# Kernel optimization log

Hardware: AMD Instinct MI355X
Metric: run time of the kernel (lower is better)

## Reference

```python
import jax, jax.numpy as jnp
import numpy as np

N = 1_000_000   # total nodes
B = 20_000      # number of graphs (segments)
V = 100_000     # item vocab (rows of feat table)
D = 128         # input_dim
H = 128         # hidden_dim
O = 256         # output_dim
EPS = 1e-5


def setup_inputs() -> dict:
    key = jax.random.key(0)
    ks = jax.random.split(key, 10)
    feat = jax.random.normal(ks[0], (V, D), dtype=jnp.float32)
    iid = jax.random.randint(ks[1], (N,), 0, V)
    segment_ids = jnp.sort(jax.random.randint(ks[2], (N,), 0, B))
    last_nodes = jax.random.randint(ks[3], (B,), 0, N)
    s = 1.0 / np.sqrt(D)
    gamma = jnp.ones((D,), jnp.float32)
    beta = jnp.zeros((D,), jnp.float32)
    W_u = jax.random.uniform(ks[4], (D, H), jnp.float32, -s, s)
    W_v = jax.random.uniform(ks[5], (D, H), jnp.float32, -s, s)
    b_v = jax.random.uniform(ks[6], (H,), jnp.float32, -s, s)
    w_e = jax.random.uniform(ks[7], (H,), jnp.float32, -1.0 / np.sqrt(H), 1.0 / np.sqrt(H))
    W_out = jax.random.uniform(ks[8], (D, O), jnp.float32, -s, s)
    return {"feat": feat, "iid": iid, "segment_ids": segment_ids,
            "last_nodes": last_nodes, "gamma": gamma, "beta": beta,
            "W_u": W_u, "W_v": W_v, "b_v": b_v, "w_e": w_e, "W_out": W_out}


def reference(feat, iid, segment_ids, last_nodes, gamma, beta, W_u, W_v, b_v, w_e, W_out):
    # gather per-node features from item table
    x = feat[iid]                                  # [N, D]
    # BatchNorm1d (training mode: batch statistics, biased var)
    mean = jnp.mean(x, axis=0)
    var = jnp.mean((x - mean) ** 2, axis=0)
    x = (x - mean) * jax.lax.rsqrt(var + EPS) * gamma + beta
    # projections
    feat_u = x @ W_u                               # [N, H]
    feat_v = x[last_nodes] @ W_v + b_v             # [B, H]
    e = jax.nn.sigmoid(feat_u + feat_v[segment_ids]) @ w_e   # [N]
    # segment softmax over per-graph node segments
    e_max = jax.ops.segment_max(e, segment_ids, num_segments=B)
    ex = jnp.exp(e - e_max[segment_ids])
    denom = jax.ops.segment_sum(ex, segment_ids, num_segments=B)
    alpha = ex / denom[segment_ids]                # [N]
    # weighted segment sum, then output projection
    rst = jax.ops.segment_sum(x * alpha[:, None], segment_ids, num_segments=B)  # [B, D]
    return rst @ W_out                             # [B, O]
```

## Files before the change

kernel.cpp:

```cpp
#include <hip/hip_runtime.h>

typedef __attribute__((ext_vector_type(8))) short short8;
typedef __attribute__((ext_vector_type(4))) float floatx4;
typedef __attribute__((ext_vector_type(4))) int intx4;

static __device__ __forceinline__ unsigned short f2bf(float x) {
    unsigned int u = __float_as_uint(x);
    u += 0x7fffu + ((u >> 16) & 1u);
    return (unsigned short)(u >> 16);
}

template <int CTRL>
static __device__ __forceinline__ float dpp_add(float x) {
    int v = __builtin_amdgcn_update_dpp(0, __float_as_int(x), CTRL, 0xf, 0xf, true);
    return x + __int_as_float(v);
}

__global__ void k_hist(const int* __restrict__ iid, int* __restrict__ counts, int N) {
    int n = blockIdx.x * blockDim.x + threadIdx.x;
    if (n < N) atomicAdd(&counts[iid[n]], 1);
}

__global__ __launch_bounds__(256) void k_cvtstats(const float* __restrict__ feat,
                                                  const int* __restrict__ counts,
                                                  unsigned short* __restrict__ featb,
                                                  float* __restrict__ dsum, float* __restrict__ dsumsq,
                                                  int V) {
    int tid = threadIdx.x;
    int r2 = tid >> 7, d = tid & 127;
    float s = 0.f, qa = 0.f;
    for (int vp = blockIdx.x; vp * 2 < V; vp += gridDim.x) {
        int v = vp * 2 + r2;
        if (v >= V) continue;
        float f = feat[(size_t)v * 128 + d];
        featb[(size_t)v * 128 + d] = f2bf(f);
        float c = (float)counts[v];
        if (c != 0.f) { s += c * f; qa += c * f * f; }
    }
    __shared__ float red[256];
    red[tid] = s; __syncthreads();
    if (tid < 128) atomicAdd(&dsum[d], red[tid] + red[tid + 128]);
    __syncthreads();
    red[tid] = qa; __syncthreads();
    if (tid < 128) atomicAdd(&dsumsq[d], red[tid] + red[tid + 128]);
}

__global__ __launch_bounds__(128) void k_affine(const float* __restrict__ sum,
                                                const float* __restrict__ sumsq,
                                                const float* __restrict__ gamma,
                                                const float* __restrict__ beta,
                                                float* __restrict__ scale, float* __restrict__ shift,
                                                float invN) {
    int d = threadIdx.x;
    float mean = sum[d] * invN;
    float var  = sumsq[d] * invN - mean * mean;
    float sc   = gamma[d] * rsqrtf(var + 1e-5f);
    scale[d] = sc;
    shift[d] = beta[d] - mean * sc;
}

__global__ __launch_bounds__(128) void k_prep(const float* __restrict__ Wu, const float* __restrict__ Wv,
                                              const float* __restrict__ bv,
                                              const float* __restrict__ scale, const float* __restrict__ shift,
                                              unsigned short* __restrict__ wut, float* __restrict__ wvs,
                                              float* __restrict__ cbias) {
    int h = blockIdx.x, d = threadIdx.x;
    float sc = scale[d], sh = shift[d];
    float wu = Wu[d * 128 + h], wv = Wv[d * 128 + h];
    wut[h * 128 + d] = f2bf(sc * wu);
    wvs[d * 128 + h] = sc * wv;
    __shared__ float red[128];
    red[d] = sh * (wu + wv);
    __syncthreads();
    for (int off = 64; off > 0; off >>= 1) {
        if (d < off) red[d] += red[d + off];
        __syncthreads();
    }
    if (d == 0) cbias[h] = bv[h] + red[0];
}

__global__ __launch_bounds__(128) void k_fv(const float* __restrict__ feat, const int* __restrict__ iid,
                                            const int* __restrict__ last, const float* __restrict__ wvs,
                                            const float* __restrict__ cbias, float* __restrict__ fv,
                                            int B) {
    const int GPB = 8;
    int b0 = blockIdx.x * GPB;
    int h = threadIdx.x;
    __shared__ float sx[GPB][128];
    for (int g = 0; g < GPB; ++g) {
        int b = b0 + g;
        if (b < B) {
            int row = iid[last[b]];
            sx[g][h] = feat[(size_t)row * 128 + h];
        }
    }
    __syncthreads();
    float acc[GPB];
#pragma unroll
    for (int g = 0; g < GPB; ++g) acc[g] = 0.f;
    for (int d = 0; d < 128; ++d) {
        float w = wvs[d * 128 + h];
#pragma unroll
        for (int g = 0; g < GPB; ++g) acc[g] += sx[g][d] * w;
    }
    float c = cbias[h];
    for (int g = 0; g < GPB; ++g)
        if (b0 + g < B) fv[(size_t)(b0 + g) * 128 + h] = acc[g] + c;
}

__global__ __launch_bounds__(256, 4) void k_main(
        const unsigned short* __restrict__ featb, const int* __restrict__ iid,
        const int* __restrict__ seg, const unsigned short* __restrict__ wut,
        const float* __restrict__ fv, const float* __restrict__ we_g,
        float* __restrict__ rstAcc, float* __restrict__ den,
        int N, int B, int numTiles) {
    __shared__ unsigned short sA[2][64 * 128];
    __shared__ int   sSeg[2][64];
    __shared__ float sFv[2][4][128];
    __shared__ float sEp[4][64];

    int tid = threadIdx.x;
    int wv = tid >> 6, lane = tid & 63, q = lane >> 4, c = lane & 15;
    int p2 = lane & 15;
    int rowbase = wv * 16 + (lane >> 4);

    short8 bfr[2][4];
    float we2[2];
#pragma unroll
    for (int t = 0; t < 2; ++t) {
        int h = (2 * wv + t) * 16 + c;
        we2[t] = we_g[h];
#pragma unroll
        for (int kc = 0; kc < 4; ++kc)
            bfr[t][kc] = *(const short8*)(wut + h * 128 + kc * 32 + q * 8);
    }

    if (blockIdx.x >= numTiles) return;

    int iidR[4]; int segR; float2 fvR;
    auto loadRegs = [&](int T) {
        int n0 = T << 6;
#pragma unroll
        for (int k = 0; k < 4; ++k)
            iidR[k] = iid[min(n0 + rowbase + 4 * k, N - 1)];
        segR = seg[min(n0 + (tid & 63), N - 1)];
        int s0 = __builtin_amdgcn_readfirstlane(segR);
        int fvrow = min(s0 + (tid >> 6), B - 1);
        fvR = *(const float2*)(fv + (size_t)fvrow * 128 + ((tid << 1) & 127));
    };
    auto stage = [&](int buf) {
        unsigned short* sAb = &sA[buf][0];
#pragma unroll
        for (int k = 0; k < 4; ++k) {
            int row = rowbase + 4 * k;
            int j = (p2 & 8) | ((p2 & 7) ^ (row & 7));
            const unsigned short* g = featb + (size_t)iidR[k] * 128 + j * 8;
            __builtin_amdgcn_global_load_lds(
                (const __attribute__((address_space(1))) void*)g,
                (__attribute__((address_space(3))) void*)(sAb + wv * 2048 + k * 512),
                16, 0, 0);
        }
        if (tid < 64) sSeg[buf][tid] = segR;
        *(float2*)&sFv[buf][tid >> 6][(tid << 1) & 127] = fvR;
    };

    int T = blockIdx.x;
    loadRegs(T);
    stage(0);
    int cur = 0;

    for (;;) {
        int Tn = T + gridDim.x;
        bool hn = (Tn < numTiles);
        if (hn) loadRegs(Tn);
        __syncthreads();
        if (hn) stage(cur ^ 1);

        floatx4 acc[4][2];
#pragma unroll
        for (int mt = 0; mt < 4; ++mt)
#pragma unroll
            for (int t = 0; t < 2; ++t) acc[mt][t] = (floatx4)(0.f);
#pragma unroll
        for (int kc = 0; kc < 4; ++kc) {
            int jj = 4 * kc + q;
            int pofs = ((jj & 8) | ((jj & 7) ^ (c & 7))) * 8;
            short8 a0 = *(const short8*)&sA[cur][( 0 + c) * 128 + pofs];
            short8 a1 = *(const short8*)&sA[cur][(16 + c) * 128 + pofs];
            short8 a2 = *(const short8*)&sA[cur][(32 + c) * 128 + pofs];
            short8 a3 = *(const short8*)&sA[cur][(48 + c) * 128 + pofs];
#pragma unroll
            for (int t = 0; t < 2; ++t) {
                acc[0][t] = __builtin_amdgcn_mfma_f32_16x16x32_bf16(a0, bfr[t][kc], acc[0][t], 0, 0, 0);
                acc[1][t] = __builtin_amdgcn_mfma_f32_16x16x32_bf16(a1, bfr[t][kc], acc[1][t], 0, 0, 0);
                acc[2][t] = __builtin_amdgcn_mfma_f32_16x16x32_bf16(a2, bfr[t][kc], acc[2][t], 0, 0, 0);
                acc[3][t] = __builtin_amdgcn_mfma_f32_16x16x32_bf16(a3, bfr[t][kc], acc[3][t], 0, 0, 0);
            }
        }
        {
            int s0 = sSeg[cur][0];
            int h0 = wv * 32 + c;
#pragma unroll
            for (int mt = 0; mt < 4; ++mt)
#pragma unroll
                for (int r = 0; r < 4; ++r) {
                    int nl = mt * 16 + q * 4 + r;
                    int sg = sSeg[cur][nl];
                    int off = sg - s0;
                    float f0, f1;
                    if (off < 4) {
                        f0 = sFv[cur][off][h0];
                        f1 = sFv[cur][off][h0 + 16];
                    } else {
                        f0 = fv[((size_t)sg << 7) + h0];
                        f1 = fv[((size_t)sg << 7) + h0 + 16];
                    }
                    float u0 = acc[mt][0][r] + f0;
                    float u1 = acc[mt][1][r] + f1;
                    float p = we2[0] * __builtin_amdgcn_rcpf(1.f + __expf(-u0))
                            + we2[1] * __builtin_amdgcn_rcpf(1.f + __expf(-u1));
                    p = dpp_add<0xb1>(p);
                    p = dpp_add<0x4e>(p);
                    p = dpp_add<0x141>(p);
                    p = dpp_add<0x140>(p);
                    if (c == 0) sEp[wv][nl] = p;
                }
        }
        __syncthreads();

        {
            int n0 = T << 6;
            int nb = wv * 16;
            float exr[16];
#pragma unroll
            for (int jg = 0; jg < 4; ++jg) {
                floatx4 e0 = *(const floatx4*)&sEp[0][nb + jg * 4];
                floatx4 e1 = *(const floatx4*)&sEp[1][nb + jg * 4];
                floatx4 e2 = *(const floatx4*)&sEp[2][nb + jg * 4];
                floatx4 e3 = *(const floatx4*)&sEp[3][nb + jg * 4];
#pragma unroll
                for (int r = 0; r < 4; ++r) {
                    float s = e0[r] + e1[r] + e2[r] + e3[r];
                    exr[jg * 4 + r] = (n0 + nb + jg * 4 + r < N) ? __expf(s) : 0.f;
                }
            }
            int sgr[16];
#pragma unroll
            for (int jg = 0; jg < 4; ++jg)
                *(intx4*)&sgr[jg * 4] = *(const intx4*)&sSeg[cur][nb + jg * 4];

            int d0 = lane * 2;
            int jj = lane >> 2;
            int wsub = (lane & 3) * 4;
            const char* base = (const char*)&sA[cur][0];
            float a0 = 0.f, a1 = 0.f, dl = 0.f;
            int curseg = sgr[0];
#pragma unroll
            for (int j = 0; j < 16; ++j) {
                int row = nb + j;
                int sg = sgr[j];
                if (sg != curseg) {
                    atomicAdd(&rstAcc[(size_t)curseg * 128 + d0], a0);
                    atomicAdd(&rstAcc[(size_t)curseg * 128 + d0 + 1], a1);
                    if (lane == 0) atomicAdd(&den[curseg], dl);
                    a0 = a1 = dl = 0.f; curseg = sg;
                }
                int ch = (jj & 8) | ((jj & 7) ^ (row & 7));
                unsigned u = *(const unsigned*)(base + row * 256 + ch * 16 + wsub);
                float e = exr[j];
                a0 += e * __uint_as_float(u << 16);
                a1 += e * __uint_as_float(u & 0xffff0000u);
                dl += e;
            }
            atomicAdd(&rstAcc[(size_t)curseg * 128 + d0], a0);
            atomicAdd(&rstAcc[(size_t)curseg * 128 + d0 + 1], a1);
            if (lane == 0) atomicAdd(&den[curseg], dl);
        }

        if (!hn) break;
        T = Tn; cur ^= 1;
    }
}

__global__ __launch_bounds__(256) void k_out(const float* __restrict__ rstAcc,
                                             const float* __restrict__ den,
                                             const float* __restrict__ scale,
                                             const float* __restrict__ shift,
                                             const float* __restrict__ Wout,
                                             float* __restrict__ out, int B) {
    __shared__ float sT[128][36];
    __shared__ float sInv[32];
    int b0 = blockIdx.x * 32;
    int t = threadIdx.x;
    for (int i = 0; i < 16; ++i) {
        int idx = i * 256 + t;
        int r = idx >> 7, d = idx & 127;
        int b = min(b0 + r, B - 1);
        sT[d][r] = scale[d] * rstAcc[((size_t)b << 7) + d];
    }
    if (t < 32) {
        int b = min(b0 + t, B - 1);
        float dn = den[b];
        sInv[t] = (dn > 0.f) ? 1.f / dn : 0.f;
    }
    __syncthreads();
    float acc[32];
#pragma unroll
    for (int r = 0; r < 32; ++r) acc[r] = 0.f;
    float sb = 0.f;
    for (int dd = 0; dd < 128; ++dd) {
        float w = Wout[dd * 256 + t];
        sb += shift[dd] * w;
        const float4* row = (const float4*)&sT[dd][0];
#pragma unroll
        for (int r4 = 0; r4 < 8; ++r4) {
            float4 v = row[r4];
            acc[r4 * 4 + 0] += w * v.x;
            acc[r4 * 4 + 1] += w * v.y;
            acc[r4 * 4 + 2] += w * v.z;
            acc[r4 * 4 + 3] += w * v.w;
        }
    }
    for (int r = 0; r < 32; ++r)
        if (b0 + r < B) {
            float inv = sInv[r];
            out[(size_t)(b0 + r) * 256 + t] = acc[r] * inv + (inv != 0.f ? sb : 0.f);
        }
}

extern "C" void kernel_launch(void* const* d_in, const int* in_sizes, int n_in,
                              void* d_out, int out_size, void* d_ws, size_t ws_size,
                              hipStream_t stream) {
    const float* feat  = (const float*)d_in[0];
    const int*   iid   = (const int*)d_in[1];
    const int*   seg   = (const int*)d_in[2];
    const int*   last  = (const int*)d_in[3];
    const float* gamma = (const float*)d_in[4];
    const float* beta  = (const float*)d_in[5];
    const float* Wu    = (const float*)d_in[6];
    const float* Wv    = (const float*)d_in[7];
    const float* bv    = (const float*)d_in[8];
    const float* we    = (const float*)d_in[9];
    const float* Wout  = (const float*)d_in[10];
    float* out = (float*)d_out;

    int V = in_sizes[0] / 128;
    int N = in_sizes[1];
    int B = in_sizes[3];

    char* w = (char*)d_ws;
    size_t off = 0;
    auto alloc = [&](size_t bytes) -> void* {
        void* p = w + off;
        off += (bytes + 255) & ~(size_t)255;
        return p;
    };
    int*   counts = (int*)alloc((size_t)V * 4);
    float* dsum   = (float*)alloc(512);
    float* dsumsq = (float*)alloc(512);
    float* rstAcc = (float*)alloc((size_t)B * 128 * 4);
    float* den    = (float*)alloc((size_t)B * 4);
    size_t zero_bytes = off;
    float* scale  = (float*)alloc(512);
    float* shift  = (float*)alloc(512);
    float* cbias  = (float*)alloc(512);
    unsigned short* wut = (unsigned short*)alloc(128 * 128 * 2);
    float* wvs    = (float*)alloc(128 * 128 * 4);
    float* fv     = (float*)alloc((size_t)B * 128 * 4);
    unsigned short* featb = (unsigned short*)alloc((size_t)V * 128 * 2);
    (void)ws_size; (void)n_in; (void)out_size;

    hipMemsetAsync(d_ws, 0, zero_bytes, stream);

    k_hist<<<(N + 255) / 256, 256, 0, stream>>>(iid, counts, N);
    k_cvtstats<<<1024, 256, 0, stream>>>(feat, counts, featb, dsum, dsumsq, V);
    k_affine<<<1, 128, 0, stream>>>(dsum, dsumsq, gamma, beta, scale, shift, 1.0f / (float)N);
    k_prep<<<128, 128, 0, stream>>>(Wu, Wv, bv, scale, shift, wut, wvs, cbias);
    k_fv<<<(B + 7) / 8, 128, 0, stream>>>(feat, iid, last, wvs, cbias, fv, B);

    int numTiles = (N + 63) / 64;
    k_main<<<1024, 256, 0, stream>>>(featb, iid, seg, wut, fv, we, rstAcc, den, N, B, numTiles);

    k_out<<<(B + 31) / 32, 256, 0, stream>>>(rstAcc, den, scale, shift, Wout, out, B);
}
```

Measured before the change: 413.8 us.

## Split main kernel tile across 8 waves with 512-thread blocks and exp2 sigmoid

Doubles the block size of the fused attention kernel to 8 waves, splitting each 64-row tile's MFMA work across two row halves so each wave holds fewer accumulators and loads fewer rows. The aim is lower register pressure and more waves in flight to hide gather latency. The sigmoid is rewritten to fold the -log2(e) factor into an FMA and use a native exp2, and the softmax/weighted-sum phase processes rows in two halves of 8 to shrink the live register set. Only 4 of the 8 waves do the segment reduction, which leaves the other half idle during that phase, and the launch changes to 768 blocks.

```diff
diff --git a/kernel.cpp b/kernel.cpp
--- a/kernel.cpp
+++ b/kernel.cpp
@@ -108,7 +108,7 @@
         if (b0 + g < B) fv[(size_t)(b0 + g) * 128 + h] = acc[g] + c;
 }
 
-__global__ __launch_bounds__(256, 4) void k_main(
+__global__ __launch_bounds__(512, 6) void k_main(
         const unsigned short* __restrict__ featb, const int* __restrict__ iid,
         const int* __restrict__ seg, const unsigned short* __restrict__ wut,
         const float* __restrict__ fv, const float* __restrict__ we_g,
@@ -119,16 +119,18 @@
     __shared__ float sFv[2][4][128];
     __shared__ float sEp[4][64];
 
+    const float NL2E = -1.44269504f;
+
     int tid = threadIdx.x;
     int wv = tid >> 6, lane = tid & 63, q = lane >> 4, c = lane & 15;
     int p2 = lane & 15;
-    int rowbase = wv * 16 + (lane >> 4);
+    int wvH = wv & 3, wvM = wv >> 2;
 
     short8 bfr[2][4];
     float we2[2];
 #pragma unroll
     for (int t = 0; t < 2; ++t) {
-        int h = (2 * wv + t) * 16 + c;
+        int h = (2 * wvH + t) * 16 + c;
         we2[t] = we_g[h];
 #pragma unroll
         for (int kc = 0; kc < 4; ++kc)
@@ -137,31 +139,31 @@
 
     if (blockIdx.x >= numTiles) return;
 
-    int iidR[4]; int segR; float2 fvR;
+    int iidR[2]; int segR; float fvR;
     auto loadRegs = [&](int T) {
         int n0 = T << 6;
 #pragma unroll
-        for (int k = 0; k < 4; ++k)
-            iidR[k] = iid[min(n0 + rowbase + 4 * k, N - 1)];
+        for (int k = 0; k < 2; ++k)
+            iidR[k] = iid[min(n0 + wv * 8 + 4 * k + (lane >> 4), N - 1)];
         segR = seg[min(n0 + (tid & 63), N - 1)];
         int s0 = __builtin_amdgcn_readfirstlane(segR);
-        int fvrow = min(s0 + (tid >> 6), B - 1);
-        fvR = *(const float2*)(fv + (size_t)fvrow * 128 + ((tid << 1) & 127));
+        int fvrow = min(s0 + (tid >> 7), B - 1);
+        fvR = NL2E * fv[(size_t)fvrow * 128 + (tid & 127)];
     };
     auto stage = [&](int buf) {
         unsigned short* sAb = &sA[buf][0];
 #pragma unroll
-        for (int k = 0; k < 4; ++k) {
-            int row = rowbase + 4 * k;
+        for (int k = 0; k < 2; ++k) {
+            int row = wv * 8 + 4 * k + (lane >> 4);
             int j = (p2 & 8) | ((p2 & 7) ^ (row & 7));
             const unsigned short* g = featb + (size_t)iidR[k] * 128 + j * 8;
             __builtin_amdgcn_global_load_lds(
                 (const __attribute__((address_space(1))) void*)g,
-                (__attribute__((address_space(3))) void*)(sAb + wv * 2048 + k * 512),
+                (__attribute__((address_space(3))) void*)(sAb + wv * 1024 + k * 512),
                 16, 0, 0);
         }
         if (tid < 64) sSeg[buf][tid] = segR;
-        *(float2*)&sFv[buf][tid >> 6][(tid << 1) & 127] = fvR;
+        sFv[buf][tid >> 7][tid & 127] = fvR;
     };
 
     int T = blockIdx.x;
@@ -176,101 +178,99 @@
         __syncthreads();
         if (hn) stage(cur ^ 1);
 
-        floatx4 acc[4][2];
-#pragma unroll
-        for (int mt = 0; mt < 4; ++mt)
+        floatx4 acc[2][2];
+#pragma unroll
+        for (int mt = 0; mt < 2; ++mt)
 #pragma unroll
             for (int t = 0; t < 2; ++t) acc[mt][t] = (floatx4)(0.f);
 #pragma unroll
         for (int kc = 0; kc < 4; ++kc) {
             int jj = 4 * kc + q;
             int pofs = ((jj & 8) | ((jj & 7) ^ (c & 7))) * 8;
-            short8 a0 = *(const short8*)&sA[cur][( 0 + c) * 128 + pofs];
-            short8 a1 = *(const short8*)&sA[cur][(16 + c) * 128 + pofs];
-            short8 a2 = *(const short8*)&sA[cur][(32 + c) * 128 + pofs];
-            short8 a3 = *(const short8*)&sA[cur][(48 + c) * 128 + pofs];
+            int rb = wvM * 32;
+            short8 a0 = *(const short8*)&sA[cur][(rb + 0  + c) * 128 + pofs];
+            short8 a1 = *(const short8*)&sA[cur][(rb + 16 + c) * 128 + pofs];
 #pragma unroll
             for (int t = 0; t < 2; ++t) {
                 acc[0][t] = __builtin_amdgcn_mfma_f32_16x16x32_bf16(a0, bfr[t][kc], acc[0][t], 0, 0, 0);
                 acc[1][t] = __builtin_amdgcn_mfma_f32_16x16x32_bf16(a1, bfr[t][kc], acc[1][t], 0, 0, 0);
-                acc[2][t] = __builtin_amdgcn_mfma_f32_16x16x32_bf16(a2, bfr[t][kc], acc[2][t], 0, 0, 0);
-                acc[3][t] = __builtin_amdgcn_mfma_f32_16x16x32_bf16(a3, bfr[t][kc], acc[3][t], 0, 0, 0);
             }
         }
         {
-            int s0 = sSeg[cur][0];
-            int h0 = wv * 32 + c;
-#pragma unroll
-            for (int mt = 0; mt < 4; ++mt)
+            int s0b = sSeg[cur][0];
+            int h0 = wvH * 32 + c;
+#pragma unroll
+            for (int mt = 0; mt < 2; ++mt)
 #pragma unroll
                 for (int r = 0; r < 4; ++r) {
-                    int nl = mt * 16 + q * 4 + r;
+                    int nl = wvM * 32 + mt * 16 + q * 4 + r;
                     int sg = sSeg[cur][nl];
-                    int off = sg - s0;
+                    int off = sg - s0b;
                     float f0, f1;
                     if (off < 4) {
                         f0 = sFv[cur][off][h0];
                         f1 = sFv[cur][off][h0 + 16];
                     } else {
-                        f0 = fv[((size_t)sg << 7) + h0];
-                        f1 = fv[((size_t)sg << 7) + h0 + 16];
+                        f0 = NL2E * fv[((size_t)sg << 7) + h0];
+                        f1 = NL2E * fv[((size_t)sg << 7) + h0 + 16];
                     }
-                    float u0 = acc[mt][0][r] + f0;
-                    float u1 = acc[mt][1][r] + f1;
-                    float p = we2[0] * __builtin_amdgcn_rcpf(1.f + __expf(-u0))
-                            + we2[1] * __builtin_amdgcn_rcpf(1.f + __expf(-u1));
+                    float m0 = __builtin_fmaf(acc[mt][0][r], NL2E, f0);
+                    float m1 = __builtin_fmaf(acc[mt][1][r], NL2E, f1);
+                    float p = we2[0] * __builtin_amdgcn_rcpf(1.f + __builtin_amdgcn_exp2f(m0))
+                            + we2[1] * __builtin_amdgcn_rcpf(1.f + __builtin_amdgcn_exp2f(m1));
                     p = dpp_add<0xb1>(p);
                     p = dpp_add<0x4e>(p);
                     p = dpp_add<0x141>(p);
                     p = dpp_add<0x140>(p);
-                    if (c == 0) sEp[wv][nl] = p;
+                    if (c == 0) sEp[wvH][nl] = p;
                 }
         }
         __syncthreads();
 
-        {
-            int n0 = T << 6;
+        if (wv < 4) {
+            int n0t = T << 6;
             int nb = wv * 16;
-            float exr[16];
-#pragma unroll
-            for (int jg = 0; jg < 4; ++jg) {
-                floatx4 e0 = *(const floatx4*)&sEp[0][nb + jg * 4];
-                floatx4 e1 = *(const floatx4*)&sEp[1][nb + jg * 4];
-                floatx4 e2 = *(const floatx4*)&sEp[2][nb + jg * 4];
-                floatx4 e3 = *(const floatx4*)&sEp[3][nb + jg * 4];
-#pragma unroll
-                for (int r = 0; r < 4; ++r) {
-                    float s = e0[r] + e1[r] + e2[r] + e3[r];
-                    exr[jg * 4 + r] = (n0 + nb + jg * 4 + r < N) ? __expf(s) : 0.f;
-                }
-            }
-            int sgr[16];
-#pragma unroll
-            for (int jg = 0; jg < 4; ++jg)
-                *(intx4*)&sgr[jg * 4] = *(const intx4*)&sSeg[cur][nb + jg * 4];
-
             int d0 = lane * 2;
             int jj = lane >> 2;
             int wsub = (lane & 3) * 4;
             const char* base = (const char*)&sA[cur][0];
             float a0 = 0.f, a1 = 0.f, dl = 0.f;
-            int curseg = sgr[0];
-#pragma unroll
-            for (int j = 0; j < 16; ++j) {
-                int row = nb + j;
-                int sg = sgr[j];
-                if (sg != curseg) {
-                    atomicAdd(&rstAcc[(size_t)curseg * 128 + d0], a0);
-                    atomicAdd(&rstAcc[(size_t)curseg * 128 + d0 + 1], a1);
-                    if (lane == 0) atomicAdd(&den[curseg], dl);
-                    a0 = a1 = dl = 0.f; curseg = sg;
+            int curseg = sSeg[cur][nb];
+#pragma unroll
+            for (int jh = 0; jh < 2; ++jh) {
+                float exr[8];
+                int sgr[8];
+#pragma unroll
+                for (int jg = 0; jg < 2; ++jg) {
+                    int rb = nb + jh * 8 + jg * 4;
+                    floatx4 e0 = *(const floatx4*)&sEp[0][rb];
+                    floatx4 e1 = *(const floatx4*)&sEp[1][rb];
+                    floatx4 e2 = *(const floatx4*)&sEp[2][rb];
+                    floatx4 e3 = *(const floatx4*)&sEp[3][rb];
+                    *(intx4*)&sgr[jg * 4] = *(const intx4*)&sSeg[cur][rb];
+#pragma unroll
+                    for (int r = 0; r < 4; ++r) {
+                        float s = e0[r] + e1[r] + e2[r] + e3[r];
+                        exr[jg * 4 + r] = (n0t + rb + r < N) ? __expf(s) : 0.f;
+                    }
                 }
-                int ch = (jj & 8) | ((jj & 7) ^ (row & 7));
-                unsigned u = *(const unsigned*)(base + row * 256 + ch * 16 + wsub);
-                float e = exr[j];
-                a0 += e * __uint_as_float(u << 16);
-                a1 += e * __uint_as_float(u & 0xffff0000u);
-                dl += e;
+#pragma unroll
+                for (int j = 0; j < 8; ++j) {
+                    int row = nb + jh * 8 + j;
+                    int sg = sgr[j];
+                    if (sg != curseg) {
+                        atomicAdd(&rstAcc[(size_t)curseg * 128 + d0], a0);
+                        atomicAdd(&rstAcc[(size_t)curseg * 128 + d0 + 1], a1);
+                        if (lane == 0) atomicAdd(&den[curseg], dl);
+                        a0 = a1 = dl = 0.f; curseg = sg;
+                    }
+                    int ch = (jj & 8) | ((jj & 7) ^ (row & 7));
+                    unsigned u = *(const unsigned*)(base + row * 256 + ch * 16 + wsub);
+                    float e = exr[j];
+                    a0 += e * __uint_as_float(u << 16);
+                    a1 += e * __uint_as_float(u & 0xffff0000u);
+                    dl += e;
+                }
             }
             atomicAdd(&rstAcc[(size_t)curseg * 128 + d0], a0);
             atomicAdd(&rstAcc[(size_t)curseg * 128 + d0 + 1], a1);
@@ -379,7 +379,7 @@
     k_fv<<<(B + 7) / 8, 128, 0, stream>>>(feat, iid, last, wvs, cbias, fv, B);
 
     int numTiles = (N + 63) / 64;
-    k_main<<<1024, 256, 0, stream>>>(featb, iid, seg, wut, fv, we, rstAcc, den, N, B, numTiles);
+    k_main<<<768, 512, 0, stream>>>(featb, iid, seg, wut, fv, we, rstAcc, den, N, B, numTiles);
 
     k_out<<<(B + 31) / 32, 256, 0, stream>>>(rstAcc, den, scale, shift, Wout, out, B);
 }
```

New measurement: 548.8 us. 32.6% more time.
